# Optimization experiments

Measured on AMD Instinct MI355X. Metric: run time of the kernel, lower is better.

The kernel has to match this reference:

```python
import jax, jax.numpy as jnp
import numpy as np

B, C, O, H, W, K, KS = 32, 128, 128, 56, 56, 4, 3
EPS = 1e-5


def setup_inputs() -> dict:
    key = jax.random.key(0)
    ks = jax.random.split(key, 6)
    sc = lambda k, shape, s: jax.random.normal(k, shape, jnp.float32) * s
    return {
        "x": jax.random.normal(ks[0], (B, C, H, W), jnp.float32),
        "fc1_w": sc(ks[1], (K, C), 0.05),
        "fc1_b": jnp.zeros((K,), jnp.float32),
        "fc2_w": sc(ks[2], (K, K), 0.3),
        "fc2_b": jnp.zeros((K,), jnp.float32),
        "weight": sc(ks[3], (K, O, C, KS, KS), 0.05),  # [K, out, in/groups, kh, kw]
        "bias": sc(ks[4], (K, O), 0.05),
        "gamma": jnp.ones((O,), jnp.float32),
        "beta": jnp.zeros((O,), jnp.float32),
    }


def reference(x, fc1_w, fc1_b, fc2_w, fc2_b, weight, bias, gamma, beta):
    # attention2d: global avg pool -> 1x1 conv (== linear) -> relu -> 1x1 conv -> softmax over K
    pooled = x.mean(axis=(2, 3))                          # [B, C]
    h = jax.nn.relu(pooled @ fc1_w.T + fc1_b)             # [B, K]
    attn = jax.nn.softmax(h @ fc2_w.T + fc2_b, axis=-1)   # [B, K]

    # per-sample aggregated kernel / bias
    agg_w = jnp.einsum('bk,koihw->boihw', attn, weight)   # [B, O, C, KS, KS]
    agg_b = attn @ bias                                    # [B, O]

    # per-sample conv (== groups=batch trick in torch)
    def conv_one(xi, wi):
        return jax.lax.conv_general_dilated(
            xi[None], wi, window_strides=(1, 1),
            padding=((1, 1), (1, 1)),
            dimension_numbers=('NCHW', 'OIHW', 'NCHW'))[0]

    out = jax.vmap(conv_one)(x, agg_w) + agg_b[:, :, None, None]  # [B, O, H, W]

    # BatchNorm2d in training mode: biased batch stats over (N, H, W)
    mean = out.mean(axis=(0, 2, 3))
    var = out.var(axis=(0, 2, 3))
    out = (out - mean[None, :, None, None]) * jax.lax.rsqrt(var + EPS)[None, :, None, None]
    out = out * gamma[None, :, None, None] + beta[None, :, None, None]
    return jax.nn.relu(out)
```

## Files before the change

kernel.cpp:

```cpp
#include <hip/hip_runtime.h>
#include <hip/hip_bf16.h>

#define BB 32
#define CC 128
#define OO 128
#define HH 56
#define WW 56
#define KK 4
#define HW 3136
#define WPLANE 147456
#define EPSV 1e-5f

#define NPOS 348
#define BUFB 22528

typedef __attribute__((ext_vector_type(8))) short short8v;
typedef __attribute__((ext_vector_type(4))) float f32x4;

static __device__ __forceinline__ void gload16(const void* g, void* l) {
    __builtin_amdgcn_global_load_lds((const __attribute__((address_space(1))) void*)g,
                                     (__attribute__((address_space(3))) void*)l, 16, 0, 0);
}

__global__ void convert_pool_kernel(const float* __restrict__ x,
                                    ushort* __restrict__ xbf,
                                    float* __restrict__ pooledp,
                                    ushort* __restrict__ zpage) {
    const int h = blockIdx.x, b = blockIdx.y;
    if (h == 0 && b == 0 && threadIdx.x < 32) zpage[threadIdx.x] = 0;
    __shared__ float4 xl4[1792];
    const float* xp = x + (size_t)(b * CC) * HW + h * WW;

    #pragma unroll
    for (int k = 0; k < 7; ++k) {
        int u = threadIdx.x + k * 256;
        int c = u / 14, w4 = u - c * 14;
        float4 v = *(const float4*)(xp + (size_t)c * HW + w4 * 4);
        xl4[u ^ ((c >> 3) & 7)] = v;
    }
    __syncthreads();

    const float* xf = (const float*)xl4;
    #pragma unroll
    for (int k = 0; k < 4; ++k) {
        int v = threadIdx.x + k * 256;
        if (v < 896) {
            int w = v >> 4, c8 = v & 15;
            int w4 = w >> 2, wo = w & 3;
            short8v res;
            #pragma unroll
            for (int j = 0; j < 8; ++j) {
                int c = c8 * 8 + j;
                int su = (c * 14 + w4) ^ (c8 & 7);
                __hip_bfloat16 hb = __float2bfloat16(xf[su * 4 + wo]);
                res[j] = *(short*)&hb;
            }
            *(short8v*)(xbf + ((size_t)((b * HH + h) * WW + w)) * CC + c8 * 8) = res;
        }
    }

    if (threadIdx.x < 128) {
        int c = threadIdx.x;
        float s = 0.f;
        #pragma unroll
        for (int w4 = 0; w4 < 14; ++w4) {
            float4 v = xl4[(c * 14 + w4) ^ ((c >> 3) & 7)];
            s += v.x + v.y + v.z + v.w;
        }
        pooledp[((size_t)(b * HH + h)) * CC + c] = s;
    }
}

__global__ void attn_aggw_kernel(const float* __restrict__ pooledp,
                                 const float* __restrict__ fc1_w, const float* __restrict__ fc1_b,
                                 const float* __restrict__ fc2_w, const float* __restrict__ fc2_b,
                                 const float* __restrict__ weight, const float* __restrict__ bias,
                                 ushort* __restrict__ aggw, float* __restrict__ agg_b) {
    const int b   = blockIdx.x / 36;
    const int rem = blockIdx.x % 36;
    const int j   = rem >> 2;
    const int ci  = rem & 3;

    __shared__ float red[8];
    __shared__ float att[4];
    const int tid = threadIdx.x;
    const int lane = tid & 63, wv = tid >> 6;

    if (tid < 128) {
        const int c = tid;
        float s = 0.f;
        for (int h = 0; h < HH; ++h) s += pooledp[((size_t)(b * HH + h)) * CC + c];
        const float pc = s * (1.0f / HW);
        #pragma unroll
        for (int k = 0; k < KK; ++k) {
            float v = pc * fc1_w[k * CC + c];
            for (int off = 32; off > 0; off >>= 1) v += __shfl_down(v, off, 64);
            if (lane == 0) red[k * 2 + wv] = v;
        }
    }
    __syncthreads();
    if (tid == 0) {
        float hk[KK], z[KK], m = -1e30f, den = 0.f;
        #pragma unroll
        for (int k = 0; k < KK; ++k)
            hk[k] = fmaxf(red[k * 2] + red[k * 2 + 1] + fc1_b[k], 0.f);
        #pragma unroll
        for (int k = 0; k < KK; ++k) {
            float t = fc2_b[k];
            #pragma unroll
            for (int jj = 0; jj < KK; ++jj) t += hk[jj] * fc2_w[k * KK + jj];
            z[k] = t; m = fmaxf(m, t);
        }
        #pragma unroll
        for (int k = 0; k < KK; ++k) { z[k] = expf(z[k] - m); den += z[k]; }
        #pragma unroll
        for (int k = 0; k < KK; ++k) att[k] = z[k] / den;
    }
    __syncthreads();
    const float a0 = att[0], a1 = att[1], a2 = att[2], a3 = att[3];

    if (rem == 0 && tid < 128) {
        const int o = tid;
        float s = 0.f;
        #pragma unroll
        for (int k = 0; k < KK; ++k) s += att[k] * bias[k * OO + o];
        agg_b[b * OO + o] = s;
    }

    ushort* op = aggw + (((size_t)b * 9 + j) * 4 + ci) * 4096;
    #pragma unroll 4
    for (int it = 0; it < 16; ++it) {
        int idx2 = tid + it * 256;
        int cc = idx2 & 31, o = idx2 >> 5;
        int c = ci * 32 + cc;
        size_t wi = ((size_t)(o * CC + c)) * 9 + j;
        float s = a0 * weight[wi]
                + a1 * weight[wi + (size_t)WPLANE]
                + a2 * weight[wi + (size_t)2*WPLANE]
                + a3 * weight[wi + (size_t)3*WPLANE];
        __hip_bfloat16 hb = __float2bfloat16(s);
        op[idx2] = *(ushort*)&hb;
    }
}

static __device__ __forceinline__ void conv_body(
        const ushort* __restrict__ xbf, const ushort* __restrict__ aggw,
        const ushort* __restrict__ zpage, ushort* xs,
        int b, int h0, int wg, int wy, int cf, int kg, int wid, int lane,
        f32x4 (&acc)[4][7]) {
    const ushort* gp[6]; int gstep[6];
    #pragma unroll
    for (int k = 0; k < 6; ++k) {
        int q = wid + 4 * k;
        int un = q * 64 + lane;
        int u = un ^ ((un >> 3) & 7);
        int pos = u >> 2, quad = u & 3;
        int row = pos / 58, col = pos - row * 58;
        int gh = h0 - 1 + row, gw = col - 1;
        bool valid = (pos < NPOS) && (gh >= 0) && (gh < HH) && (gw >= 0) && (gw < WW);
        gp[k] = valid ? (xbf + ((size_t)((b * HH + gh) * WW + gw)) * CC + quad * 8) : zpage;
        gstep[k] = valid ? 32 : 0;
    }

    int blin[7];
    #pragma unroll
    for (int nf = 0; nf < 7; ++nf) {
        int p = wy * 112 + nf * 16 + cf;
        int r = p / 56, w = p - r * 56;
        blin[nf] = (((r + 1) * 58 + (w + 1)) << 6) + kg * 16;
    }

    const ushort* Ab = aggw + ((size_t)b * 36) * 4096 + (size_t)(wg * 64 + cf) * 32 + kg * 8;
    #define ALOAD(mf_, j_, ci_) (*(const short8v*)(Ab + (size_t)((j_) * 4 + (ci_)) * 4096 + (mf_) * 512))

    short8v paA[4], paB[4];
    #pragma unroll
    for (int mf = 0; mf < 4; ++mf) paA[mf] = ALOAD(mf, 0, 0);
    #pragma unroll
    for (int mf = 0; mf < 4; ++mf) paB[mf] = ALOAD(mf, 1, 0);

    #pragma unroll
    for (int k = 0; k < 6; ++k) {
        int q = wid + 4 * k;
        if (q < 22) { gload16(gp[k], (char*)xs + q * 1024); gp[k] += gstep[k]; }
    }
    __syncthreads();

    int cur = 0;
    for (int ci = 0; ci < 4; ++ci) {
        if (ci < 3) {
            char* base = (char*)xs + (cur ^ 1) * BUFB;
            #pragma unroll
            for (int k = 0; k < 6; ++k) {
                int q = wid + 4 * k;
                if (q < 22) { gload16(gp[k], base + q * 1024); gp[k] += gstep[k]; }
            }
        }
        const char* xbuf = (const char*)xs + cur * BUFB;

        short8v bfc[7], bfn[7];
        #pragma unroll
        for (int nf = 0; nf < 7; ++nf) {
            int lin = blin[nf] + (-58 - 1) * 64;
            int swz = lin ^ ((lin >> 3) & 0x70);
            bfc[nf] = *(const short8v*)(xbuf + swz);
        }
        #pragma unroll
        for (int j = 0; j < 9; ++j) {
            if (j < 8) {
                const int toff = (((j+1)/3 - 1) * 58 + ((j+1)%3 - 1)) * 64;
                #pragma unroll
                for (int nf = 0; nf < 7; ++nf) {
                    int lin = blin[nf] + toff;
                    int swz = lin ^ ((lin >> 3) & 0x70);
                    bfn[nf] = *(const short8v*)(xbuf + swz);
                }
            }
            short8v ca[4];
            #pragma unroll
            for (int mf = 0; mf < 4; ++mf) { ca[mf] = paA[mf]; paA[mf] = paB[mf]; }
            const int f = j + 2;
            if (f < 9) {
                #pragma unroll
                for (int mf = 0; mf < 4; ++mf) paB[mf] = ALOAD(mf, f, ci);
            } else if (ci < 3) {
                #pragma unroll
                for (int mf = 0; mf < 4; ++mf) paB[mf] = ALOAD(mf, f - 9, ci + 1);
            }
            #pragma unroll
            for (int nf = 0; nf < 7; ++nf) {
                #pragma unroll
                for (int mf = 0; mf < 4; ++mf)
                    acc[mf][nf] = __builtin_amdgcn_mfma_f32_16x16x32_bf16(ca[mf], bfc[nf], acc[mf][nf], 0, 0, 0);
            }
            if (j < 8) {
                #pragma unroll
                for (int nf = 0; nf < 7; ++nf) bfc[nf] = bfn[nf];
            }
        }
        if (ci < 3) __syncthreads();
        cur ^= 1;
    }
    #undef ALOAD
}

template <bool BF16OUT>
__launch_bounds__(256, 2)
__global__ void conv_kernel(const ushort* __restrict__ xbf, const ushort* __restrict__ aggw,
                            const float* __restrict__ agg_b, const ushort* __restrict__ zpage,
                            void* __restrict__ outv,
                            float* __restrict__ psum, float* __restrict__ psumsq) {
    const int lid  = blockIdx.x;
    const int gwid = (lid & 7) * 56 + (lid >> 3);
    const int b = gwid / 14;
    const int t = gwid - b * 14;
    const int h0 = t * 4;
    __shared__ ushort xs[2 * BUFB / 2];

    const int tid  = threadIdx.x;
    const int lane = tid & 63;
    const int wid  = tid >> 6;
    const int wg = wid & 1, wy = wid >> 1;
    const int cf = lane & 15, kg = lane >> 4;

    f32x4 acc[4][7];
    #pragma unroll
    for (int mf = 0; mf < 4; ++mf)
        #pragma unroll
        for (int nf = 0; nf < 7; ++nf) acc[mf][nf] = (f32x4){0.f, 0.f, 0.f, 0.f};

    conv_body(xbf, aggw, zpage, xs, b, h0, wg, wy, cf, kg, wid, lane, acc);

    #pragma unroll
    for (int mf = 0; mf < 4; ++mf) {
        #pragma unroll
        for (int i = 0; i < 4; ++i) {
            const int o = wg * 64 + mf * 16 + kg * 4 + i;
            const float ab = agg_b[b * OO + o];
            const size_t obase = ((size_t)(b * OO + o)) * HW;
            float s = 0.f, s2 = 0.f;
            #pragma unroll
            for (int nf = 0; nf < 7; ++nf) {
                int p = wy * 112 + nf * 16 + cf;
                int r = p / 56, w = p - r * 56;
                float v = acc[mf][nf][i] + ab;
                if (BF16OUT) {
                    __hip_bfloat16 hb = __float2bfloat16(v);
                    ((ushort*)outv)[obase + (h0 + r) * WW + w] = *(ushort*)&hb;
                } else {
                    ((float*)outv)[obase + (h0 + r) * WW + w] = v;
                }
                s += v; s2 += v * v;
            }
            s  += __shfl_xor(s, 1, 64);  s  += __shfl_xor(s, 2, 64);
            s  += __shfl_xor(s, 4, 64);  s  += __shfl_xor(s, 8, 64);
            s2 += __shfl_xor(s2, 1, 64); s2 += __shfl_xor(s2, 2, 64);
            s2 += __shfl_xor(s2, 4, 64); s2 += __shfl_xor(s2, 8, 64);
            if (cf == 0) {
                int row = (b * 14 + t) * 2 + wy;
                psum[o * 896 + row]   = s;
                psumsq[o * 896 + row] = s2;
            }
        }
    }
}

template <bool BF16IN>
__global__ void bn2_kernel(const void* __restrict__ src, float* __restrict__ out,
                           const float* __restrict__ psum, const float* __restrict__ psumsq,
                           const float* __restrict__ gamma, const float* __restrict__ beta) {
    const int o  = blockIdx.x & 127;
    const int bg = blockIdx.x >> 7;
    const int tid = threadIdx.x;
    const int lane = tid & 63, wv = tid >> 6;
    __shared__ float red[8];
    __shared__ float par[2];

    float s = 0.f, s2 = 0.f;
    for (int r = tid; r < 896; r += 256) {
        s  += psum[o * 896 + r];
        s2 += psumsq[o * 896 + r];
    }
    for (int off = 32; off > 0; off >>= 1) {
        s  += __shfl_down(s, off, 64);
        s2 += __shfl_down(s2, off, 64);
    }
    if (lane == 0) { red[wv] = s; red[4 + wv] = s2; }
    __syncthreads();
    if (tid == 0) {
        const float invN = 1.0f / (float)(BB * HW);
        float S  = red[0] + red[1] + red[2] + red[3];
        float S2 = red[4] + red[5] + red[6] + red[7];
        float mean = S * invN;
        float var  = S2 * invN - mean * mean;
        float inv  = rsqrtf(var + EPSV);
        par[0] = gamma[o] * inv;
        par[1] = beta[o] - mean * par[0];
    }
    __syncthreads();
    const float g = par[0], bt = par[1];

    #pragma unroll
    for (int b2 = 0; b2 < 4; ++b2) {
        const int b = bg * 4 + b2;
        const size_t base = ((size_t)(b * OO + o)) * HW;
        for (int u = tid; u < 392; u += 256) {
            float4 lo, hi;
            if (BF16IN) {
                short8v v = *(const short8v*)((const ushort*)src + base + u * 8);
                #pragma unroll
                for (int jj = 0; jj < 4; ++jj) {
                    ushort uu = (ushort)v[jj];
                    ((float*)&lo)[jj] = fmaxf(__bfloat162float(*(__hip_bfloat16*)&uu) * g + bt, 0.f);
                }
                #pragma unroll
                for (int jj = 0; jj < 4; ++jj) {
                    ushort uu = (ushort)v[4 + jj];
                    ((float*)&hi)[jj] = fmaxf(__bfloat162float(*(__hip_bfloat16*)&uu) * g + bt, 0.f);
                }
            } else {
                float4 v0 = *(const float4*)((const float*)src + base + u * 8);
                float4 v1 = *(const float4*)((const float*)src + base + u * 8 + 4);
                lo.x = fmaxf(v0.x * g + bt, 0.f); lo.y = fmaxf(v0.y * g + bt, 0.f);
                lo.z = fmaxf(v0.z * g + bt, 0.f); lo.w = fmaxf(v0.w * g + bt, 0.f);
                hi.x = fmaxf(v1.x * g + bt, 0.f); hi.y = fmaxf(v1.y * g + bt, 0.f);
                hi.z = fmaxf(v1.z * g + bt, 0.f); hi.w = fmaxf(v1.w * g + bt, 0.f);
            }
            *(float4*)(out + base + u * 8)     = lo;
            *(float4*)(out + base + u * 8 + 4) = hi;
        }
    }
}

extern "C" void kernel_launch(void* const* d_in, const int* in_sizes, int n_in,
                              void* d_out, int out_size, void* d_ws, size_t ws_size,
                              hipStream_t stream) {
    const float* x      = (const float*)d_in[0];
    const float* fc1_w  = (const float*)d_in[1];
    const float* fc1_b  = (const float*)d_in[2];
    const float* fc2_w  = (const float*)d_in[3];
    const float* fc2_b  = (const float*)d_in[4];
    const float* weight = (const float*)d_in[5];
    const float* bias   = (const float*)d_in[6];
    const float* gamma  = (const float*)d_in[7];
    const float* beta   = (const float*)d_in[8];
    float* out = (float*)d_out;

    const size_t XBF_ELEMS  = (size_t)BB * HW * CC;
    const size_t AGGW_ELEMS = (size_t)BB * 9 * OO * CC;
    const size_t OUT_ELEMS  = (size_t)BB * OO * HW;
    ushort* xbf  = (ushort*)d_ws;
    ushort* aggw = xbf + XBF_ELEMS;
    float*  wsf  = (float*)(aggw + AGGW_ELEMS);
    float* pooledp = wsf;
    float* attn    = pooledp + 229376;
    float* agg_b   = attn + 128;
    float* psum    = agg_b + 4096;
    float* psumsq  = psum + 114688;
    float* sums    = psumsq + 114688;
    float* sumsq   = sums + 128;
    ushort* zpage  = (ushort*)(sumsq + 128);
    ushort* convout = (ushort*)(zpage + 32);

    const size_t need = (size_t)((char*)(convout + OUT_ELEMS) - (char*)d_ws);
    const bool bf16path = ws_size >= need;

    convert_pool_kernel<<<dim3(HH, BB), 256, 0, stream>>>(x, xbf, pooledp, zpage);
    attn_aggw_kernel<<<dim3(1152), 256, 0, stream>>>(pooledp, fc1_w, fc1_b, fc2_w, fc2_b,
                                                     weight, bias, aggw, agg_b);
    if (bf16path) {
        conv_kernel<true><<<dim3(448), 256, 0, stream>>>(xbf, aggw, agg_b, zpage,
                                                         (void*)convout, psum, psumsq);
        bn2_kernel<true><<<dim3(1024), 256, 0, stream>>>((const void*)convout, out,
                                                         psum, psumsq, gamma, beta);
    } else {
        conv_kernel<false><<<dim3(448), 256, 0, stream>>>(xbf, aggw, agg_b, zpage,
                                                          (void*)out, psum, psumsq);
        bn2_kernel<false><<<dim3(1024), 256, 0, stream>>>((const void*)out, out,
                                                          psum, psumsq, gamma, beta);
    }
}
```

Baseline: 105.2 us.

## Process four rows per convert block and shorten weight prefetch depth

The convert/pool kernel now handles four image rows per block and stages them in LDS as bf16 rather than fp32, with a 57-stride swizzled layout. This cuts the grid from 56x32 to 14x32 blocks and reduces the partial-sum count fed to the attention kernel. Because pooling now sums the bf16-rounded values, the attention input loses some precision. The conv kernel's A-operand prefetch drops from two steps ahead to one, freeing registers at the cost of less latency hiding, and unused workspace buffers are removed.

```diff
diff --git a/kernel.cpp b/kernel.cpp
--- a/kernel.cpp
+++ b/kernel.cpp
@@ -26,48 +26,59 @@
                                     ushort* __restrict__ xbf,
                                     float* __restrict__ pooledp,
                                     ushort* __restrict__ zpage) {
-    const int h = blockIdx.x, b = blockIdx.y;
-    if (h == 0 && b == 0 && threadIdx.x < 32) zpage[threadIdx.x] = 0;
-    __shared__ float4 xl4[1792];
-    const float* xp = x + (size_t)(b * CC) * HW + h * WW;
-
-    #pragma unroll
-    for (int k = 0; k < 7; ++k) {
-        int u = threadIdx.x + k * 256;
-        int c = u / 14, w4 = u - c * 14;
-        float4 v = *(const float4*)(xp + (size_t)c * HW + w4 * 4);
-        xl4[u ^ ((c >> 3) & 7)] = v;
-    }
-    __syncthreads();
-
-    const float* xf = (const float*)xl4;
-    #pragma unroll
-    for (int k = 0; k < 4; ++k) {
-        int v = threadIdx.x + k * 256;
-        if (v < 896) {
-            int w = v >> 4, c8 = v & 15;
-            int w4 = w >> 2, wo = w & 3;
-            short8v res;
-            #pragma unroll
-            for (int j = 0; j < 8; ++j) {
-                int c = c8 * 8 + j;
-                int su = (c * 14 + w4) ^ (c8 & 7);
-                __hip_bfloat16 hb = __float2bfloat16(xf[su * 4 + wo]);
-                res[j] = *(short*)&hb;
-            }
-            *(short8v*)(xbf + ((size_t)((b * HH + h) * WW + w)) * CC + c8 * 8) = res;
-        }
-    }
-
-    if (threadIdx.x < 128) {
-        int c = threadIdx.x;
+    const int hq = blockIdx.x;
+    const int b  = blockIdx.y;
+    const int h0 = hq * 4;
+    if (hq == 0 && b == 0 && threadIdx.x < 32) zpage[threadIdx.x] = 0;
+    __shared__ ushort xl[128 * 57 * 4];
+    const float* xb = x + (size_t)(b * CC) * HW + h0 * WW;
+    const int tid = threadIdx.x;
+
+    #pragma unroll
+    for (int k = 0; k < 28; ++k) {
+        int u = tid + k * 256;
+        int c = u / 56, i = u - c * 56;
+        float4 v = *(const float4*)(xb + (size_t)c * HW + i * 4);
+        ushort4 r;
+        __hip_bfloat16 b0 = __float2bfloat16(v.x);
+        __hip_bfloat16 b1 = __float2bfloat16(v.y);
+        __hip_bfloat16 b2 = __float2bfloat16(v.z);
+        __hip_bfloat16 b3 = __float2bfloat16(v.w);
+        r.x = *(ushort*)&b0; r.y = *(ushort*)&b1;
+        r.z = *(ushort*)&b2; r.w = *(ushort*)&b3;
+        *(ushort4*)(&xl[(c * 57 + (i ^ ((c >> 3) & 7))) * 4]) = r;
+    }
+    __syncthreads();
+
+    #pragma unroll
+    for (int k = 0; k < 14; ++k) {
+        int v = tid + k * 256;
+        int row = v / 896, rem = v - row * 896;
+        int w = rem >> 4, c8 = rem & 15;
+        int i = row * 14 + (w >> 2);
+        int e = w & 3;
+        short8v r;
+        #pragma unroll
+        for (int j = 0; j < 8; ++j) {
+            int c = c8 * 8 + j;
+            r[j] = (short)xl[(c * 57 + (i ^ (c8 & 7))) * 4 + e];
+        }
+        *(short8v*)(xbf + ((size_t)((b * HH + h0 + row) * WW + w)) * CC + c8 * 8) = r;
+    }
+
+    if (tid < 128) {
+        const int c = tid;
         float s = 0.f;
         #pragma unroll
-        for (int w4 = 0; w4 < 14; ++w4) {
-            float4 v = xl4[(c * 14 + w4) ^ ((c >> 3) & 7)];
-            s += v.x + v.y + v.z + v.w;
-        }
-        pooledp[((size_t)(b * HH + h)) * CC + c] = s;
+        for (int i = 0; i < 56; ++i) {
+            const ushort* q = &xl[(c * 57 + (i ^ ((c >> 3) & 7))) * 4];
+            #pragma unroll
+            for (int e = 0; e < 4; ++e) {
+                ushort u = q[e];
+                s += __bfloat162float(*(__hip_bfloat16*)&u);
+            }
+        }
+        pooledp[((size_t)(b * 14 + hq)) * CC + c] = s;
     }
 }
 
@@ -89,7 +100,8 @@
     if (tid < 128) {
         const int c = tid;
         float s = 0.f;
-        for (int h = 0; h < HH; ++h) s += pooledp[((size_t)(b * HH + h)) * CC + c];
+        #pragma unroll
+        for (int h = 0; h < 14; ++h) s += pooledp[((size_t)(b * 14 + h)) * CC + c];
         const float pc = s * (1.0f / HW);
         #pragma unroll
         for (int k = 0; k < KK; ++k) {
@@ -173,11 +185,9 @@
     const ushort* Ab = aggw + ((size_t)b * 36) * 4096 + (size_t)(wg * 64 + cf) * 32 + kg * 8;
     #define ALOAD(mf_, j_, ci_) (*(const short8v*)(Ab + (size_t)((j_) * 4 + (ci_)) * 4096 + (mf_) * 512))
 
-    short8v paA[4], paB[4];
-    #pragma unroll
-    for (int mf = 0; mf < 4; ++mf) paA[mf] = ALOAD(mf, 0, 0);
-    #pragma unroll
-    for (int mf = 0; mf < 4; ++mf) paB[mf] = ALOAD(mf, 1, 0);
+    short8v pa[4];
+    #pragma unroll
+    for (int mf = 0; mf < 4; ++mf) pa[mf] = ALOAD(mf, 0, 0);
 
     #pragma unroll
     for (int k = 0; k < 6; ++k) {
@@ -218,14 +228,13 @@
             }
             short8v ca[4];
             #pragma unroll
-            for (int mf = 0; mf < 4; ++mf) { ca[mf] = paA[mf]; paA[mf] = paB[mf]; }
-            const int f = j + 2;
-            if (f < 9) {
-                #pragma unroll
-                for (int mf = 0; mf < 4; ++mf) paB[mf] = ALOAD(mf, f, ci);
+            for (int mf = 0; mf < 4; ++mf) ca[mf] = pa[mf];
+            if (j < 8) {
+                #pragma unroll
+                for (int mf = 0; mf < 4; ++mf) pa[mf] = ALOAD(mf, j + 1, ci);
             } else if (ci < 3) {
                 #pragma unroll
-                for (int mf = 0; mf < 4; ++mf) paB[mf] = ALOAD(mf, f - 9, ci + 1);
+                for (int mf = 0; mf < 4; ++mf) pa[mf] = ALOAD(mf, 0, ci + 1);
             }
             #pragma unroll
             for (int nf = 0; nf < 7; ++nf) {
@@ -393,19 +402,16 @@
     ushort* aggw = xbf + XBF_ELEMS;
     float*  wsf  = (float*)(aggw + AGGW_ELEMS);
     float* pooledp = wsf;
-    float* attn    = pooledp + 229376;
-    float* agg_b   = attn + 128;
+    float* agg_b   = pooledp + 57344;
     float* psum    = agg_b + 4096;
     float* psumsq  = psum + 114688;
-    float* sums    = psumsq + 114688;
-    float* sumsq   = sums + 128;
-    ushort* zpage  = (ushort*)(sumsq + 128);
+    ushort* zpage  = (ushort*)(psumsq + 114688);
     ushort* convout = (ushort*)(zpage + 32);
 
     const size_t need = (size_t)((char*)(convout + OUT_ELEMS) - (char*)d_ws);
     const bool bf16path = ws_size >= need;
 
-    convert_pool_kernel<<<dim3(HH, BB), 256, 0, stream>>>(x, xbf, pooledp, zpage);
+    convert_pool_kernel<<<dim3(14, BB), 256, 0, stream>>>(x, xbf, pooledp, zpage);
     attn_aggw_kernel<<<dim3(1152), 256, 0, stream>>>(pooledp, fc1_w, fc1_b, fc2_w, fc2_b,
                                                      weight, bias, aggw, agg_b);
     if (bf16path) {
```

After: 97.41 us (median of 2 runs). 7.4% less time.
